# Optimization experiments

Hardware: AMD Instinct MI355X
Metric: run time of the kernel (lower is better)

Reference implementation:

```python
import jax, jax.numpy as jnp
import numpy as np

N = 50000
E = 800000
IN_C = 128
HID = 32
HEADS = 8
OUT_C = 64
NEG_SLOPE = 0.2


def setup_inputs() -> dict:
    key = jax.random.key(0)
    ks = jax.random.split(key, 12)
    x = jax.random.normal(ks[0], (N, IN_C), dtype=jnp.float32)
    edge_index = jax.random.randint(ks[1], (2, E), 0, N, dtype=jnp.int64)
    s = 0.05
    W1 = jax.random.normal(ks[2], (IN_C, HEADS * HID), dtype=jnp.float32) * s
    a1_src = jax.random.normal(ks[3], (HEADS, HID), dtype=jnp.float32) * s
    a1_dst = jax.random.normal(ks[4], (HEADS, HID), dtype=jnp.float32) * s
    b1 = jnp.zeros((HEADS * HID,), dtype=jnp.float32)
    W2 = jax.random.normal(ks[5], (HEADS * HID, OUT_C), dtype=jnp.float32) * s
    a2_src = jax.random.normal(ks[6], (1, OUT_C), dtype=jnp.float32) * s
    a2_dst = jax.random.normal(ks[7], (1, OUT_C), dtype=jnp.float32) * s
    b2 = jnp.zeros((OUT_C,), dtype=jnp.float32)
    return {"x": x, "edge_index": edge_index, "W1": W1, "a1_src": a1_src,
            "a1_dst": a1_dst, "b1": b1, "W2": W2, "a2_src": a2_src,
            "a2_dst": a2_dst, "b2": b2}


def gat_conv(x, W, a_src, a_dst, bias, src, dst, concat):
    # x: [N, F_in]; W: [F_in, H*C]; a_src/a_dst: [H, C]
    H, C = a_src.shape
    h = (x @ W).reshape(N, H, C)                      # [N, H, C]
    alpha_s = jnp.einsum('nhc,hc->nh', h, a_src)      # [N, H]
    alpha_d = jnp.einsum('nhc,hc->nh', h, a_dst)
    e = alpha_s[src] + alpha_d[dst]                   # [E, H]
    e = jnp.where(e >= 0, e, NEG_SLOPE * e)           # leaky relu
    # segment softmax over destination nodes
    m = jax.ops.segment_max(e, dst, num_segments=N)   # [N, H]
    e = jnp.exp(e - m[dst])
    z = jax.ops.segment_sum(e, dst, num_segments=N)   # [N, H]
    alpha = e / z[dst]                                # [E, H]
    msg = h[src] * alpha[:, :, None]                  # [E, H, C]
    out = jax.ops.segment_sum(msg, dst, num_segments=N)  # [N, H, C]
    if concat:
        out = out.reshape(N, H * C)
    else:
        out = out.mean(axis=1)
    return out + bias


def reference(x, edge_index, W1, a1_src, a1_dst, b1, W2, a2_src, a2_dst, b2):
    src, dst = edge_index[0], edge_index[1]
    # dropout omitted (eval mode)
    h = gat_conv(x, W1, a1_src, a1_dst, b1, src, dst, concat=True)
    h = jax.nn.elu(h)
    out = gat_conv(h, W2, a2_src, a2_dst, b2, src, dst, concat=False)
    return out
```

## Files before the change

kernel.cpp:

```cpp
#include <hip/hip_runtime.h>
#include <cstdint>
#include <cstddef>

#define N_NODES 50000
#define N_EDGES 800000
#define INC 128
#define HID 32
#define HEADS 8
#define OUTC 64
#define F1 (HEADS * HID)
#define NEG 0.2f
#define CAP 64

typedef unsigned short bf16_t;
typedef unsigned short u16;
typedef __attribute__((ext_vector_type(8))) short bf16x8;
typedef __attribute__((ext_vector_type(4))) float f32x4;

__device__ __forceinline__ float bf2f(bf16_t u) {
  union { unsigned int i; float f; } v;
  v.i = ((unsigned int)u) << 16;
  return v.f;
}
__device__ __forceinline__ bf16_t f2bf(float x) {
  union { float f; unsigned int u; } v;
  v.f = x;
  unsigned int r = v.u + 0x7FFFu + ((v.u >> 16) & 1u);
  return (bf16_t)(r >> 16);
}
__device__ __forceinline__ float lrexp(float v) {
  return expf((v >= 0.f) ? v : NEG * v);
}

__global__ __launch_bounds__(256) void prep(
    const float* __restrict__ x, const float* __restrict__ W1,
    const float* __restrict__ W2, bf16_t* __restrict__ xb,
    bf16_t* __restrict__ W1T, bf16_t* __restrict__ W2T,
    const int* __restrict__ srcE, const int* __restrict__ dstE,
    int* __restrict__ cnt, u16* __restrict__ bucket) {
  int t = blockIdx.x * 256 + threadIdx.x;
  if (t < N_EDGES) {
    int dd = dstE[t];
    int pos = atomicAdd(&cnt[dd], 1);
    bucket[(size_t)dd * CAP + pos] = (u16)srcE[t];
  }
  if (t < (N_NODES * INC) / 8) {
    const float4* xp = reinterpret_cast<const float4*>(x + (size_t)t * 8);
    float4 v0 = xp[0], v1 = xp[1];
    union { bf16_t h[8]; uint4 u; } pk;
    pk.h[0] = f2bf(v0.x); pk.h[1] = f2bf(v0.y);
    pk.h[2] = f2bf(v0.z); pk.h[3] = f2bf(v0.w);
    pk.h[4] = f2bf(v1.x); pk.h[5] = f2bf(v1.y);
    pk.h[6] = f2bf(v1.z); pk.h[7] = f2bf(v1.w);
    *reinterpret_cast<uint4*>(xb + (size_t)t * 8) = pk.u;
  }
  if (t < INC * F1) {
    int k = t >> 8, n = t & 255;
    W1T[(size_t)n * INC + k] = f2bf(W1[t]);
  }
  if (t < F1 * OUTC) {
    int k = t >> 6, n = t & 63;
    W2T[(size_t)n * F1 + k] = f2bf(W2[t]);
  }
}

template <int KV, int NT, int HPT, int HTOT>
__global__ __launch_bounds__(256) void mfma_gemm(
    const bf16_t* __restrict__ A16, const bf16_t* __restrict__ Wt,
    bf16_t* __restrict__ C, const float* __restrict__ a_src,
    const float* __restrict__ a_dst, float* __restrict__ as,
    float* __restrict__ ad, int M) {
  constexpr int N = NT * 64;
  constexpr int NCH = KV / 8;
  constexpr int KK = KV / 32;
  __shared__ union SM {
    bf16_t A[64 * KV];
    struct { float ct[64][65]; float pr[64][4]; } epi;
  } sm;

  const int tid = threadIdx.x;
  const int wave = tid >> 6, lane = tid & 63;
  const int wm = (wave >> 1) * 32, wn = (wave & 1) * 32;
  const int lr = lane & 15, lq = lane >> 4;
  const int m0 = blockIdx.x * 64;

  {
    constexpr int ITER = 64 * NCH / 256;
#pragma unroll
    for (int q = 0; q < ITER; q++) {
      int id = q * 256 + tid;
      int r = id / NCH, c = id % NCH;
      int gm = m0 + r;
      uint4 v = make_uint4(0, 0, 0, 0);
      if (gm < M) v = *reinterpret_cast<const uint4*>(&A16[(size_t)gm * KV + c * 8]);
      *reinterpret_cast<uint4*>(&sm.A[r * KV + ((c ^ (r & 7)) * 8)]) = v;
    }
  }
  __syncthreads();

  f32x4 acc[NT][2][2];
#pragma unroll
  for (int n = 0; n < NT; n++)
#pragma unroll
    for (int mi = 0; mi < 2; mi++)
#pragma unroll
      for (int ni = 0; ni < 2; ni++)
        acc[n][mi][ni] = (f32x4){0.f, 0.f, 0.f, 0.f};

  auto loadB = [&](int n, bf16x8 (&b)[KK][2]) {
    const int n0 = n * 64;
#pragma unroll
    for (int ni = 0; ni < 2; ni++) {
      const size_t brow = (size_t)(n0 + wn + ni * 16 + lr) * KV;
#pragma unroll
      for (int kk = 0; kk < KK; kk++)
        b[kk][ni] = *reinterpret_cast<const bf16x8*>(&Wt[brow + kk * 32 + lq * 8]);
    }
  };

  bf16x8 bcur[KK][2], bnxt[KK][2];
  loadB(0, bcur);
#pragma unroll
  for (int n = 0; n < NT; n++) {
    if (n + 1 < NT) loadB(n + 1, bnxt);
#pragma unroll
    for (int kk = 0; kk < KK; kk++) {
      bf16x8 af[2];
#pragma unroll
      for (int mi = 0; mi < 2; mi++) {
        int rr = wm + mi * 16 + lr;
        af[mi] = *reinterpret_cast<const bf16x8*>(
            &sm.A[rr * KV + (((kk * 4 + lq) ^ (rr & 7)) * 8)]);
      }
#pragma unroll
      for (int mi = 0; mi < 2; mi++)
#pragma unroll
        for (int ni = 0; ni < 2; ni++)
          acc[n][mi][ni] = __builtin_amdgcn_mfma_f32_16x16x32_bf16(
              af[mi], bcur[kk][ni], acc[n][mi][ni], 0, 0, 0);
    }
    if (n + 1 < NT) {
#pragma unroll
      for (int kk = 0; kk < KK; kk++)
#pragma unroll
        for (int ni = 0; ni < 2; ni++)
          bcur[kk][ni] = bnxt[kk][ni];
    }
  }
  __syncthreads();

#pragma unroll
  for (int n = 0; n < NT; n++) {
    const int n0 = n * 64;
#pragma unroll
    for (int mi = 0; mi < 2; mi++)
#pragma unroll
      for (int ni = 0; ni < 2; ni++)
#pragma unroll
        for (int r = 0; r < 4; r++)
          sm.epi.ct[wm + mi * 16 + lq * 4 + r][wn + ni * 16 + lr] = acc[n][mi][ni][r];
    __syncthreads();

    {
      int row = tid >> 2, ch = tid & 3;
      int gm = m0 + row;
      if (gm < M) {
        union { bf16_t h[8]; uint4 u; } pk0, pk1;
#pragma unroll
        for (int c = 0; c < 8; c++) pk0.h[c] = f2bf(sm.epi.ct[row][ch * 16 + c]);
#pragma unroll
        for (int c = 0; c < 8; c++) pk1.h[c] = f2bf(sm.epi.ct[row][ch * 16 + 8 + c]);
        *reinterpret_cast<uint4*>(&C[(size_t)gm * N + n0 + ch * 16]) = pk0.u;
        *reinterpret_cast<uint4*>(&C[(size_t)gm * N + n0 + ch * 16 + 8]) = pk1.u;
      }
    }

    {
      int row = tid >> 2, part = tid & 3;
      int gn = m0 + row;
      const float* av = ((part & 2) ? a_dst : a_src) + n0 + (part & 1) * 32;
      float dot = 0.f;
#pragma unroll
      for (int c = 0; c < 32; c++) dot += sm.epi.ct[row][(part & 1) * 32 + c] * av[c];
      if constexpr (HPT == 2) {
        if (gn < M) {
          float* tgt = (part & 2) ? ad : as;
          tgt[(size_t)gn * HTOT + (n0 >> 5) + (part & 1)] = dot;
        }
      } else {
        sm.epi.pr[row][part] = dot;
        __syncthreads();
        if (part == 0 && gn < M) {
          as[gn] = sm.epi.pr[row][0] + sm.epi.pr[row][1];
          ad[gn] = sm.epi.pr[row][2] + sm.epi.pr[row][3];
        }
      }
    }
    __syncthreads();
  }
}

__global__ __launch_bounds__(256) void gat_aggr1(
    const int* __restrict__ cnt, const u16* __restrict__ bucket,
    const float* __restrict__ as, const float* __restrict__ ad,
    const bf16_t* __restrict__ hb, const float* __restrict__ bias,
    bf16_t* __restrict__ outp) {
  int d = blockIdx.x * 4 + (threadIdx.x >> 6);
  int lane = threadIdx.x & 63;
  if (d >= N_NODES) return;
  int deg = cnt[d];
  const u16* bkt = bucket + (size_t)d * CAP;
  const int sh = lane & 7;
  const int es = lane >> 3;
  const int ah = lane >> 3;
  float ad_h = ad[(size_t)d * 8 + sh];
  float a0 = 0.f, a1 = 0.f, a2 = 0.f, a3 = 0.f, zacc = 0.f;

  if (deg > 0) {
    int ei = es;
    int s_reg = (int)bkt[(ei < deg) ? ei : deg - 1];
    float w_reg = (ei < deg) ? lrexp(as[(size_t)s_reg * 8 + sh] + ad_h) : 0.f;

    for (int cb = 0; cb < deg; cb += 8) {
      const bf16_t* bs[8];
#pragma unroll
      for (int e = 0; e < 8; e++)
        bs[e] = hb + (size_t)__builtin_amdgcn_readlane(s_reg, e << 3) * F1;
      uint2 g[8];
#pragma unroll
      for (int e = 0; e < 8; e++)
        g[e] = *reinterpret_cast<const uint2*>(bs[e] + 4 * lane);
      float w_cur = w_reg;
      zacc += w_reg;
      int nxt = cb + 8;
      if (nxt < deg) {
        int ei2 = nxt + es;
        s_reg = (int)bkt[(ei2 < deg) ? ei2 : deg - 1];
        w_reg = (ei2 < deg) ? lrexp(as[(size_t)s_reg * 8 + sh] + ad_h) : 0.f;
      }
#pragma unroll
      for (int e = 0; e < 8; e++) {
        float wv = __shfl(w_cur, (e << 3) | ah);
        union { uint2 u; bf16_t h[4]; } ld;
        ld.u = g[e];
        a0 += bf2f(ld.h[0]) * wv;
        a1 += bf2f(ld.h[1]) * wv;
        a2 += bf2f(ld.h[2]) * wv;
        a3 += bf2f(ld.h[3]) * wv;
      }
    }
  }

  float zr = zacc;
  zr += __shfl_xor(zr, 8);
  zr += __shfl_xor(zr, 16);
  zr += __shfl_xor(zr, 32);
  float z = __shfl(zr, ah);

  float inv = (deg > 0) ? (1.f / z) : 0.f;
  float4 bv = *reinterpret_cast<const float4*>(&bias[4 * lane]);
  float v0 = a0 * inv + bv.x;
  float v1 = a1 * inv + bv.y;
  float v2 = a2 * inv + bv.z;
  float v3 = a3 * inv + bv.w;
  v0 = (v0 > 0.f) ? v0 : expm1f(v0);
  v1 = (v1 > 0.f) ? v1 : expm1f(v1);
  v2 = (v2 > 0.f) ? v2 : expm1f(v2);
  v3 = (v3 > 0.f) ? v3 : expm1f(v3);
  union { bf16_t h[4]; uint2 u; } pk;
  pk.h[0] = f2bf(v0); pk.h[1] = f2bf(v1); pk.h[2] = f2bf(v2); pk.h[3] = f2bf(v3);
  *reinterpret_cast<uint2*>(&outp[(size_t)d * F1 + 4 * lane]) = pk.u;
}

__global__ __launch_bounds__(256) void gat_aggr2(
    const int* __restrict__ cnt, const u16* __restrict__ bucket,
    const float* __restrict__ as, const float* __restrict__ ad,
    const bf16_t* __restrict__ hb, const float* __restrict__ bias,
    float* __restrict__ outp) {
  int d = blockIdx.x * 32 + (threadIdx.x >> 3);
  int sub = threadIdx.x & 7;
  if (d >= N_NODES) return;
  int deg = cnt[d];
  const u16* bkt = bucket + (size_t)d * CAP;
  float ad_d = ad[d];
  float acc[8] = {};
  float zacc = 0.f;

  if (deg > 0) {
    int ei = sub;
    int s_reg = (int)bkt[(ei < deg) ? ei : deg - 1];
    float w_reg = (ei < deg) ? lrexp(as[s_reg] + ad_d) : 0.f;

    for (int cb = 0; cb < deg; cb += 8) {
      int sv[8];
#pragma unroll
      for (int e = 0; e < 8; e++) sv[e] = __shfl(s_reg, e, 8);
      uint4 g[8];
#pragma unroll
      for (int e = 0; e < 8; e++)
        g[e] = *reinterpret_cast<const uint4*>(&hb[(size_t)sv[e] * OUTC + 8 * sub]);
      float w_cur = w_reg;
      zacc += w_reg;
      int nxt = cb + 8;
      if (nxt < deg) {
        int ei2 = nxt + sub;
        s_reg = (int)bkt[(ei2 < deg) ? ei2 : deg - 1];
        w_reg = (ei2 < deg) ? lrexp(as[s_reg] + ad_d) : 0.f;
      }
#pragma unroll
      for (int e = 0; e < 8; e++) {
        float wv = __shfl(w_cur, e, 8);
        union { uint4 u; bf16_t h[8]; } ld;
        ld.u = g[e];
#pragma unroll
        for (int q = 0; q < 8; q++) acc[q] += bf2f(ld.h[q]) * wv;
      }
    }
  }

  float zr = zacc;
  zr += __shfl_xor(zr, 1, 8);
  zr += __shfl_xor(zr, 2, 8);
  zr += __shfl_xor(zr, 4, 8);

  float inv = (deg > 0) ? (1.f / zr) : 0.f;
  float4 o0, o1;
  o0.x = acc[0] * inv + bias[8 * sub + 0];
  o0.y = acc[1] * inv + bias[8 * sub + 1];
  o0.z = acc[2] * inv + bias[8 * sub + 2];
  o0.w = acc[3] * inv + bias[8 * sub + 3];
  o1.x = acc[4] * inv + bias[8 * sub + 4];
  o1.y = acc[5] * inv + bias[8 * sub + 5];
  o1.z = acc[6] * inv + bias[8 * sub + 6];
  o1.w = acc[7] * inv + bias[8 * sub + 7];
  *reinterpret_cast<float4*>(&outp[(size_t)d * OUTC + 8 * sub]) = o0;
  *reinterpret_cast<float4*>(&outp[(size_t)d * OUTC + 8 * sub + 4]) = o1;
}

extern "C" void kernel_launch(void* const* d_in, const int* in_sizes, int n_in,
                              void* d_out, int out_size, void* d_ws, size_t ws_size,
                              hipStream_t stream) {
  const float* x      = (const float*)d_in[0];
  const int*   ei     = (const int*)d_in[1];
  const float* W1     = (const float*)d_in[2];
  const float* a1_src = (const float*)d_in[3];
  const float* a1_dst = (const float*)d_in[4];
  const float* b1     = (const float*)d_in[5];
  const float* W2     = (const float*)d_in[6];
  const float* a2_src = (const float*)d_in[7];
  const float* a2_dst = (const float*)d_in[8];
  const float* b2     = (const float*)d_in[9];

  const int* src = ei;
  const int* dst = ei + N_EDGES;
  float* out = (float*)d_out;

  char* base = (char*)d_ws;
  size_t off = 0;
  auto carve = [&](size_t bytes) {
    void* q = base + off;
    off += (bytes + 255) & ~size_t(255);
    return q;
  };
  bf16_t* h1b  = (bf16_t*)carve((size_t)N_NODES * F1 * 2);
  bf16_t* o1b  = (bf16_t*)carve((size_t)N_NODES * F1 * 2);
  float* as1 = (float*)carve((size_t)N_NODES * HEADS * 4);
  float* ad1 = (float*)carve((size_t)N_NODES * HEADS * 4);
  float* as2 = (float*)carve((size_t)N_NODES * 4);
  float* ad2 = (float*)carve((size_t)N_NODES * 4);
  int* cnt = (int*)carve((size_t)N_NODES * 4);
  u16* bucket = (u16*)carve((size_t)N_NODES * CAP * 2);
  bf16_t* w1t = (bf16_t*)carve((size_t)F1 * INC * 2);
  bf16_t* w2t = (bf16_t*)carve((size_t)OUTC * F1 * 2);
  bf16_t* xb  = (bf16_t*)carve((size_t)N_NODES * INC * 2);
  bf16_t* h2b = h1b;

  hipMemsetAsync(cnt, 0, N_NODES * sizeof(int), stream);
  prep<<<(N_EDGES + 255) / 256, 256, 0, stream>>>(
      x, W1, W2, xb, w1t, w2t, src, dst, cnt, bucket);

  mfma_gemm<INC, F1 / 64, 2, HEADS><<<(N_NODES + 63) / 64, 256, 0, stream>>>(
      xb, w1t, h1b, a1_src, a1_dst, as1, ad1, N_NODES);

  gat_aggr1<<<(N_NODES + 3) / 4, 256, 0, stream>>>(cnt, bucket, as1, ad1, h1b, b1, o1b);

  mfma_gemm<F1, OUTC / 64, 1, 1><<<(N_NODES + 63) / 64, 256, 0, stream>>>(
      o1b, w2t, h2b, a2_src, a2_dst, as2, ad2, N_NODES);

  gat_aggr2<<<(N_NODES + 31) / 32, 256, 0, stream>>>(cnt, bucket, as2, ad2, h2b, b2, out);
}
```

Before: 263.1 us.

## Use head-major layer-1 features, per-head aggregation blocks, and fuse bucketing into GEMM

After: 375.7 us. +42.8%, slower.

```diff
diff --git a/kernel.cpp b/kernel.cpp
--- a/kernel.cpp
+++ b/kernel.cpp
@@ -35,15 +35,8 @@
 __global__ __launch_bounds__(256) void prep(
     const float* __restrict__ x, const float* __restrict__ W1,
     const float* __restrict__ W2, bf16_t* __restrict__ xb,
-    bf16_t* __restrict__ W1T, bf16_t* __restrict__ W2T,
-    const int* __restrict__ srcE, const int* __restrict__ dstE,
-    int* __restrict__ cnt, u16* __restrict__ bucket) {
+    bf16_t* __restrict__ W1T, bf16_t* __restrict__ W2T, int* __restrict__ cnt) {
   int t = blockIdx.x * 256 + threadIdx.x;
-  if (t < N_EDGES) {
-    int dd = dstE[t];
-    int pos = atomicAdd(&cnt[dd], 1);
-    bucket[(size_t)dd * CAP + pos] = (u16)srcE[t];
-  }
   if (t < (N_NODES * INC) / 8) {
     const float4* xp = reinterpret_cast<const float4*>(x + (size_t)t * 8);
     float4 v0 = xp[0], v1 = xp[1];
@@ -54,6 +47,7 @@
     pk.h[6] = f2bf(v1.z); pk.h[7] = f2bf(v1.w);
     *reinterpret_cast<uint4*>(xb + (size_t)t * 8) = pk.u;
   }
+  if (t < N_NODES) cnt[t] = 0;
   if (t < INC * F1) {
     int k = t >> 8, n = t & 255;
     W1T[(size_t)n * INC + k] = f2bf(W1[t]);
@@ -64,12 +58,14 @@
   }
 }
 
-template <int KV, int NT, int HPT, int HTOT>
+template <int KV, int NT, int HPT, bool CHM>
 __global__ __launch_bounds__(256) void mfma_gemm(
     const bf16_t* __restrict__ A16, const bf16_t* __restrict__ Wt,
     bf16_t* __restrict__ C, const float* __restrict__ a_src,
     const float* __restrict__ a_dst, float* __restrict__ as,
-    float* __restrict__ ad, int M) {
+    float* __restrict__ ad, int M,
+    const int* __restrict__ srcE, const int* __restrict__ dstE,
+    int* __restrict__ cnt, u16* __restrict__ bucket) {
   constexpr int N = NT * 64;
   constexpr int NCH = KV / 8;
   constexpr int KK = KV / 32;
@@ -79,6 +75,15 @@
   } sm;
 
   const int tid = threadIdx.x;
+
+  if (cnt != nullptr) {
+    for (int e = blockIdx.x * 256 + tid; e < N_EDGES; e += gridDim.x * 256) {
+      int dd = dstE[e];
+      int pos = atomicAdd(&cnt[dd], 1);
+      bucket[(size_t)dd * CAP + pos] = (u16)srcE[e];
+    }
+  }
+
   const int wave = tid >> 6, lane = tid & 63;
   const int wm = (wave >> 1) * 32, wn = (wave & 1) * 32;
   const int lr = lane & 15, lq = lane >> 4;
@@ -170,8 +175,16 @@
         for (int c = 0; c < 8; c++) pk0.h[c] = f2bf(sm.epi.ct[row][ch * 16 + c]);
 #pragma unroll
         for (int c = 0; c < 8; c++) pk1.h[c] = f2bf(sm.epi.ct[row][ch * 16 + 8 + c]);
-        *reinterpret_cast<uint4*>(&C[(size_t)gm * N + n0 + ch * 16]) = pk0.u;
-        *reinterpret_cast<uint4*>(&C[(size_t)gm * N + n0 + ch * 16 + 8]) = pk1.u;
+        if constexpr (CHM) {
+          int hh = (n0 >> 5) + (ch >> 1);
+          size_t base = (size_t)hh * ((size_t)N_NODES * HID) +
+                        (size_t)gm * HID + (ch & 1) * 16;
+          *reinterpret_cast<uint4*>(&C[base]) = pk0.u;
+          *reinterpret_cast<uint4*>(&C[base + 8]) = pk1.u;
+        } else {
+          *reinterpret_cast<uint4*>(&C[(size_t)gm * N + n0 + ch * 16]) = pk0.u;
+          *reinterpret_cast<uint4*>(&C[(size_t)gm * N + n0 + ch * 16 + 8]) = pk1.u;
+        }
       }
     }
 
@@ -185,7 +198,7 @@
       if constexpr (HPT == 2) {
         if (gn < M) {
           float* tgt = (part & 2) ? ad : as;
-          tgt[(size_t)gn * HTOT + (n0 >> 5) + (part & 1)] = dot;
+          tgt[(size_t)((n0 >> 5) + (part & 1)) * N_NODES + gn] = dot;
         }
       } else {
         sm.epi.pr[row][part] = dot;
@@ -200,76 +213,69 @@
   }
 }
 
-__global__ __launch_bounds__(256) void gat_aggr1(
+__global__ __launch_bounds__(512) void gat_aggr1(
     const int* __restrict__ cnt, const u16* __restrict__ bucket,
     const float* __restrict__ as, const float* __restrict__ ad,
     const bf16_t* __restrict__ hb, const float* __restrict__ bias,
     bf16_t* __restrict__ outp) {
-  int d = blockIdx.x * 4 + (threadIdx.x >> 6);
-  int lane = threadIdx.x & 63;
+  const int h = blockIdx.x & 7;
+  const int d = (blockIdx.x >> 3) * 8 + (threadIdx.x >> 6);
+  const int lane = threadIdx.x & 63;
   if (d >= N_NODES) return;
-  int deg = cnt[d];
-  const u16* bkt = bucket + (size_t)d * CAP;
-  const int sh = lane & 7;
-  const int es = lane >> 3;
-  const int ah = lane >> 3;
-  float ad_h = ad[(size_t)d * 8 + sh];
-  float a0 = 0.f, a1 = 0.f, a2 = 0.f, a3 = 0.f, zacc = 0.f;
+  const int deg = cnt[d];
+  const int sl = lane >> 3;
+  const int fl = lane & 7;
+  const bf16_t* __restrict__ hbh = hb + (size_t)h * ((size_t)N_NODES * HID);
+
+  float a0 = 0.f, a1 = 0.f, a2 = 0.f, a3 = 0.f, z = 0.f;
 
   if (deg > 0) {
-    int ei = es;
-    int s_reg = (int)bkt[(ei < deg) ? ei : deg - 1];
-    float w_reg = (ei < deg) ? lrexp(as[(size_t)s_reg * 8 + sh] + ad_h) : 0.f;
-
+    const u16* bkt = bucket + (size_t)d * CAP;
+    float ad_h = ad[(size_t)h * N_NODES + d];
+    int idx = (lane < deg) ? lane : deg - 1;
+    int s_all = (int)bkt[idx];
+    float w_all = (lane < deg)
+        ? lrexp(as[(size_t)h * N_NODES + s_all] + ad_h) : 0.f;
+    float zr = w_all;
+    zr += __shfl_xor(zr, 1);
+    zr += __shfl_xor(zr, 2);
+    zr += __shfl_xor(zr, 4);
+    zr += __shfl_xor(zr, 8);
+    zr += __shfl_xor(zr, 16);
+    zr += __shfl_xor(zr, 32);
+    z = zr;
     for (int cb = 0; cb < deg; cb += 8) {
-      const bf16_t* bs[8];
-#pragma unroll
-      for (int e = 0; e < 8; e++)
-        bs[e] = hb + (size_t)__builtin_amdgcn_readlane(s_reg, e << 3) * F1;
-      uint2 g[8];
-#pragma unroll
-      for (int e = 0; e < 8; e++)
-        g[e] = *reinterpret_cast<const uint2*>(bs[e] + 4 * lane);
-      float w_cur = w_reg;
-      zacc += w_reg;
-      int nxt = cb + 8;
-      if (nxt < deg) {
-        int ei2 = nxt + es;
-        s_reg = (int)bkt[(ei2 < deg) ? ei2 : deg - 1];
-        w_reg = (ei2 < deg) ? lrexp(as[(size_t)s_reg * 8 + sh] + ad_h) : 0.f;
-      }
-#pragma unroll
-      for (int e = 0; e < 8; e++) {
-        float wv = __shfl(w_cur, (e << 3) | ah);
-        union { uint2 u; bf16_t h[4]; } ld;
-        ld.u = g[e];
-        a0 += bf2f(ld.h[0]) * wv;
-        a1 += bf2f(ld.h[1]) * wv;
-        a2 += bf2f(ld.h[2]) * wv;
-        a3 += bf2f(ld.h[3]) * wv;
-      }
-    }
-  }
-
-  float zr = zacc;
-  zr += __shfl_xor(zr, 8);
-  zr += __shfl_xor(zr, 16);
-  zr += __shfl_xor(zr, 32);
-  float z = __shfl(zr, ah);
-
-  float inv = (deg > 0) ? (1.f / z) : 0.f;
-  float4 bv = *reinterpret_cast<const float4*>(&bias[4 * lane]);
-  float v0 = a0 * inv + bv.x;
-  float v1 = a1 * inv + bv.y;
-  float v2 = a2 * inv + bv.z;
-  float v3 = a3 * inv + bv.w;
-  v0 = (v0 > 0.f) ? v0 : expm1f(v0);
-  v1 = (v1 > 0.f) ? v1 : expm1f(v1);
-  v2 = (v2 > 0.f) ? v2 : expm1f(v2);
-  v3 = (v3 > 0.f) ? v3 : expm1f(v3);
-  union { bf16_t h[4]; uint2 u; } pk;
-  pk.h[0] = f2bf(v0); pk.h[1] = f2bf(v1); pk.h[2] = f2bf(v2); pk.h[3] = f2bf(v3);
-  *reinterpret_cast<uint2*>(&outp[(size_t)d * F1 + 4 * lane]) = pk.u;
+      int src = __shfl(s_all, cb + sl);
+      float wv = __shfl(w_all, cb + sl);
+      union { uint2 u; bf16_t hh[4]; } ld;
+      ld.u = *reinterpret_cast<const uint2*>(&hbh[(size_t)src * HID + fl * 4]);
+      a0 += bf2f(ld.hh[0]) * wv;
+      a1 += bf2f(ld.hh[1]) * wv;
+      a2 += bf2f(ld.hh[2]) * wv;
+      a3 += bf2f(ld.hh[3]) * wv;
+    }
+    a0 += __shfl_xor(a0, 8); a0 += __shfl_xor(a0, 16); a0 += __shfl_xor(a0, 32);
+    a1 += __shfl_xor(a1, 8); a1 += __shfl_xor(a1, 16); a1 += __shfl_xor(a1, 32);
+    a2 += __shfl_xor(a2, 8); a2 += __shfl_xor(a2, 16); a2 += __shfl_xor(a2, 32);
+    a3 += __shfl_xor(a3, 8); a3 += __shfl_xor(a3, 16); a3 += __shfl_xor(a3, 32);
+  }
+
+  if (lane < 8) {
+    float inv = (deg > 0) ? (1.f / z) : 0.f;
+    float4 bv = *reinterpret_cast<const float4*>(&bias[h * HID + lane * 4]);
+    float v0 = a0 * inv + bv.x;
+    float v1 = a1 * inv + bv.y;
+    float v2 = a2 * inv + bv.z;
+    float v3 = a3 * inv + bv.w;
+    v0 = (v0 > 0.f) ? v0 : expm1f(v0);
+    v1 = (v1 > 0.f) ? v1 : expm1f(v1);
+    v2 = (v2 > 0.f) ? v2 : expm1f(v2);
+    v3 = (v3 > 0.f) ? v3 : expm1f(v3);
+    union { bf16_t hh[4]; uint2 u; } pk;
+    pk.hh[0] = f2bf(v0); pk.hh[1] = f2bf(v1);
+    pk.hh[2] = f2bf(v2); pk.hh[3] = f2bf(v3);
+    *reinterpret_cast<uint2*>(&outp[(size_t)d * F1 + h * HID + lane * 4]) = pk.u;
+  }
 }
 
 __global__ __launch_bounds__(256) void gat_aggr2(
@@ -375,17 +381,18 @@
   bf16_t* xb  = (bf16_t*)carve((size_t)N_NODES * INC * 2);
   bf16_t* h2b = h1b;
 
-  hipMemsetAsync(cnt, 0, N_NODES * sizeof(int), stream);
-  prep<<<(N_EDGES + 255) / 256, 256, 0, stream>>>(
-      x, W1, W2, xb, w1t, w2t, src, dst, cnt, bucket);
-
-  mfma_gemm<INC, F1 / 64, 2, HEADS><<<(N_NODES + 63) / 64, 256, 0, stream>>>(
-      xb, w1t, h1b, a1_src, a1_dst, as1, ad1, N_NODES);
-
-  gat_aggr1<<<(N_NODES + 3) / 4, 256, 0, stream>>>(cnt, bucket, as1, ad1, h1b, b1, o1b);
-
-  mfma_gemm<F1, OUTC / 64, 1, 1><<<(N_NODES + 63) / 64, 256, 0, stream>>>(
-      o1b, w2t, h2b, a2_src, a2_dst, as2, ad2, N_NODES);
+  prep<<<(N_NODES * INC / 8 + 255) / 256, 256, 0, stream>>>(
+      x, W1, W2, xb, w1t, w2t, cnt);
+
+  mfma_gemm<INC, F1 / 64, 2, true><<<(N_NODES + 63) / 64, 256, 0, stream>>>(
+      xb, w1t, h1b, a1_src, a1_dst, as1, ad1, N_NODES, src, dst, cnt, bucket);
+
+  gat_aggr1<<<8 * ((N_NODES + 7) / 8), 512, 0, stream>>>(
+      cnt, bucket, as1, ad1, h1b, b1, o1b);
+
+  mfma_gemm<F1, OUTC / 64, 1, false><<<(N_NODES + 63) / 64, 256, 0, stream>>>(
+      o1b, w2t, h2b, a2_src, a2_dst, as2, ad2, N_NODES,
+      nullptr, nullptr, nullptr, nullptr);
 
   gat_aggr2<<<(N_NODES + 31) / 32, 256, 0, stream>>>(cnt, bucket, as2, ad2, h2b, b2, out);
 }
```
